# Performance work log

Hardware: AMD Instinct MI355X
Metric: run time of the kernel (lower is better)

## Reference

```python
import jax, jax.numpy as jnp
import numpy as np

VAR = 1.0
STD = float(np.sqrt(VAR))


def setup_inputs() -> dict:
    key = jax.random.key(0)
    k1, k2 = jax.random.split(key)
    n, c = 262144, 100
    scores = jax.random.normal(k1, (n, c), dtype=jnp.float32)
    labels = jax.random.randint(k2, (n,), 0, c, dtype=jnp.int64)
    return {"scores": scores, "labels": labels}


def reference(scores, labels):
    n, c = scores.shape
    # Gaussian pdf over class indices, centered at each label (re_encode_label)
    x = jnp.arange(c, dtype=scores.dtype)[None, :]            # (1, c)
    mu = labels.astype(scores.dtype)[:, None]                  # (n, 1)
    inv_norm = 1.0 / (STD * np.sqrt(2.0 * np.pi))
    code = inv_norm * jnp.exp(-0.5 * ((x - mu) / STD) ** 2)    # (n, c)
    # target distribution: softmax over the (unnormalized) pdf values
    target = jax.nn.softmax(code, axis=1)
    logsfmx = jax.nn.log_softmax(scores, axis=1)
    # KLDivLoss(reduction='batchmean'): sum(target * (log target - input)) / n
    kl = jnp.sum(target * (jnp.log(target) - logsfmx)) / n
    return kl
```

## Files before the change

kernel.cpp:

```cpp
#include <hip/hip_runtime.h>
#include <math.h>

#define C 100
#define WAVES 4
#define ROWS_PER_PASS 32
#define PASSES 4
#define ROWS_PER_BLOCK (ROWS_PER_PASS * PASSES)
#define PASS_FLOATS (ROWS_PER_PASS * C)
#define FULL_CHUNKS 12
#define INV_NORM 0.3989422804014327f
#define WFAR     0.67102943f

__device__ __forceinline__ float quad_sum(float x) {
    x += __int_as_float(__builtin_amdgcn_update_dpp(
            0, __float_as_int(x), 0xB1, 0xF, 0xF, true));
    x += __int_as_float(__builtin_amdgcn_update_dpp(
            0, __float_as_int(x), 0x4E, 0xF, 0xF, true));
    return x;
}
__device__ __forceinline__ float oct_sum(float x) {
    x = quad_sum(x);
    x += __shfl_xor(x, 4);
    return x;
}

__global__ __launch_bounds__(256, 6) void kl_main(
    const float* __restrict__ scores,
    const int*   __restrict__ labels,
    float* __restrict__ out, int n, float inv_n)
{
    __shared__ float buf[2][PASS_FLOATS];
    __shared__ float wpart[WAVES];

    const int tid  = threadIdx.x;
    const int wave = tid >> 6, lane = tid & 63;
    const int rw   = lane >> 3;
    const int sub8 = lane & 7;
    const int rowInPassBase = wave * 8 + rw;

    const int blockRow0 = blockIdx.x * ROWS_PER_BLOCK;
    const size_t totalBytes = (size_t)n * C * 4;

    int mu[PASSES];
    #pragma unroll
    for (int p = 0; p < PASSES; ++p) {
        int row = blockRow0 + p * ROWS_PER_PASS + rowInPassBase;
        mu[p] = (row < n) ? labels[row] : 0;
    }

    float acc = 0.f;

    auto stage = [&](int p, int b) {
        const size_t byteBase = (size_t)(blockRow0 + p * ROWS_PER_PASS) * (C * 4);
        #pragma unroll
        for (int k = 0; k < 3; ++k) {
            int c = wave + k * WAVES;
            size_t off = byteBase + (size_t)c * 1024;
            if (off + 1024 > totalBytes) off = totalBytes - 1024;
            const char* src = (const char*)scores + off + lane * 16;
            __builtin_amdgcn_global_load_lds(
                (const __attribute__((address_space(1))) void*)src,
                (__attribute__((address_space(3))) void*)&buf[b][c * 256],
                16, 0, 0);
        }
        if (wave == 0) {
            size_t off = byteBase + (size_t)FULL_CHUNKS * 1024;
            if (off + 512 > totalBytes) off = totalBytes - 512;
            if (lane < 32) {
                const char* src = (const char*)scores + off + lane * 16;
                __builtin_amdgcn_global_load_lds(
                    (const __attribute__((address_space(1))) void*)src,
                    (__attribute__((address_space(3))) void*)&buf[b][FULL_CHUNKS * 256],
                    16, 0, 0);
            }
        }
    };

    auto consume = [&](int p, int b) {
        const float* sp = &buf[b][rowInPassBase * C];
        const int off = sub8 * 13 - max(sub8 - 4, 0);
        const float* spl = sp + off;
        float se = 0.f, rs = 0.f;
        #pragma unroll
        for (int i = 0; i < 12; ++i) {
            float s = spl[i];
            se += __expf(s);
            rs += s;
        }
        if (sub8 < 4) {
            float s = spl[12];
            se += __expf(s);
            rs += s;
        }
        se = oct_sum(se);
        rs = oct_sum(rs);

        const float WP[7] = {0.32897057f, 0.18369895f, 0.03722540f,
            0.00298049f, 8.9804e-5f, 9.9763e-7f, 4.0768e-9f};
        const float WC[7] = {0.39894228f, 0.20681926f, 0.03823936f,
            0.00298711f, 8.9816e-5f, 9.9765e-7f, 4.0768e-9f};
        float dotw = 0.f, csum = 100.f * WFAR, dotc = 0.f;
        const int m = mu[p];
        #pragma unroll
        for (int d = -6; d <= 6; ++d) {
            int idx  = m + d;
            bool ok  = (unsigned)idx < (unsigned)C;
            float s  = sp[min(max(idx, 0), C - 1)];
            int a    = d < 0 ? -d : d;
            float wv = ok ? WP[a] : 0.f;
            dotw  = fmaf(wv, s, dotw);
            csum += wv;
            dotc += ok ? WC[a] : 0.f;
        }

        int myrow = blockRow0 + p * ROWS_PER_PASS + rowInPassBase;
        if (sub8 == 0 && myrow < n) {
            float dot = fmaf(WFAR, rs, dotw);
            acc += (dotc - dot) / csum - INV_NORM - __logf(csum) + __logf(se);
        }
    };

    #define VMBAR(N) do { asm volatile("s_waitcnt vmcnt(" #N ")" ::: "memory"); \
                          __builtin_amdgcn_s_barrier();                          \
                          asm volatile("" ::: "memory"); } while (0)
    #define BAR()    do { asm volatile("" ::: "memory");                         \
                          __builtin_amdgcn_s_barrier();                          \
                          asm volatile("" ::: "memory"); } while (0)

    stage(0, 0);
    stage(1, 1);

    VMBAR(3);
    consume(0, 0);
    BAR();
    stage(2, 0);

    VMBAR(3);
    consume(1, 1);
    BAR();
    stage(3, 1);

    VMBAR(3);
    consume(2, 0);

    VMBAR(0);
    consume(3, 1);

    #undef VMBAR
    #undef BAR

    #pragma unroll
    for (int off = 32; off > 0; off >>= 1)
        acc += __shfl_xor(acc, off, 64);
    if (lane == 0) wpart[wave] = acc;
    __syncthreads();
    if (tid == 0)
        atomicAdd(out, (wpart[0] + wpart[1] + wpart[2] + wpart[3]) * inv_n);
}

extern "C" void kernel_launch(void* const* d_in, const int* in_sizes, int n_in,
                              void* d_out, int out_size, void* d_ws, size_t ws_size,
                              hipStream_t stream)
{
    const float* scores = (const float*)d_in[0];
    const int*   labels = (const int*)d_in[1];
    float*       out    = (float*)d_out;

    int n = in_sizes[0] / C;

    hipMemsetAsync(d_out, 0, sizeof(float) * (size_t)out_size, stream);

    int blocks = (n + ROWS_PER_BLOCK - 1) / ROWS_PER_BLOCK;
    kl_main<<<blocks, 256, 0, stream>>>(scores, labels, out, n, 1.0f / (float)n);
}
```

Measured before the change: 164.6 us.

## Double rows per block and generalize LDS double-buffer pipeline loop

Doubles the number of 32-row passes per block from 4 to 8, so each block handles 256 rows and the grid shrinks by half, which spreads the per-block prologue and atomic cost over more work. The hand-unrolled stage/consume sequence becomes a generic unrolled loop. The wait count is now per wave, since wave 0 issues an extra tail load. The out-of-bounds clamping on global addresses is removed, which assumes n is a multiple of the block row count; otherwise the last block would read past the end of the array.

```diff
diff --git a/kernel.cpp b/kernel.cpp
--- a/kernel.cpp
+++ b/kernel.cpp
@@ -4,7 +4,7 @@
 #define C 100
 #define WAVES 4
 #define ROWS_PER_PASS 32
-#define PASSES 4
+#define PASSES 8
 #define ROWS_PER_BLOCK (ROWS_PER_PASS * PASSES)
 #define PASS_FLOATS (ROWS_PER_PASS * C)
 #define FULL_CHUNKS 12
@@ -39,7 +39,6 @@
     const int rowInPassBase = wave * 8 + rw;
 
     const int blockRow0 = blockIdx.x * ROWS_PER_BLOCK;
-    const size_t totalBytes = (size_t)n * C * 4;
 
     int mu[PASSES];
     #pragma unroll
@@ -55,24 +54,20 @@
         #pragma unroll
         for (int k = 0; k < 3; ++k) {
             int c = wave + k * WAVES;
-            size_t off = byteBase + (size_t)c * 1024;
-            if (off + 1024 > totalBytes) off = totalBytes - 1024;
-            const char* src = (const char*)scores + off + lane * 16;
+            const char* src = (const char*)scores + byteBase + (size_t)c * 1024
+                              + lane * 16;
             __builtin_amdgcn_global_load_lds(
                 (const __attribute__((address_space(1))) void*)src,
                 (__attribute__((address_space(3))) void*)&buf[b][c * 256],
                 16, 0, 0);
         }
-        if (wave == 0) {
-            size_t off = byteBase + (size_t)FULL_CHUNKS * 1024;
-            if (off + 512 > totalBytes) off = totalBytes - 512;
-            if (lane < 32) {
-                const char* src = (const char*)scores + off + lane * 16;
-                __builtin_amdgcn_global_load_lds(
-                    (const __attribute__((address_space(1))) void*)src,
-                    (__attribute__((address_space(3))) void*)&buf[b][FULL_CHUNKS * 256],
-                    16, 0, 0);
-            }
+        if (wave == 0 && lane < 32) {
+            const char* src = (const char*)scores + byteBase
+                              + (size_t)FULL_CHUNKS * 1024 + lane * 16;
+            __builtin_amdgcn_global_load_lds(
+                (const __attribute__((address_space(1))) void*)src,
+                (__attribute__((address_space(3))) void*)&buf[b][FULL_CHUNKS * 256],
+                16, 0, 0);
         }
     };
 
@@ -120,34 +115,29 @@
         }
     };
 
-    #define VMBAR(N) do { asm volatile("s_waitcnt vmcnt(" #N ")" ::: "memory"); \
-                          __builtin_amdgcn_s_barrier();                          \
-                          asm volatile("" ::: "memory"); } while (0)
-    #define BAR()    do { asm volatile("" ::: "memory");                         \
-                          __builtin_amdgcn_s_barrier();                          \
-                          asm volatile("" ::: "memory"); } while (0)
-
     stage(0, 0);
     stage(1, 1);
 
-    VMBAR(3);
-    consume(0, 0);
-    BAR();
-    stage(2, 0);
+    #pragma unroll
+    for (int p = 0; p < PASSES; ++p) {
+        if (p < PASSES - 1) {
+            if (wave == 0) asm volatile("s_waitcnt vmcnt(4)" ::: "memory");
+            else           asm volatile("s_waitcnt vmcnt(3)" ::: "memory");
+        } else {
+            asm volatile("s_waitcnt vmcnt(0)" ::: "memory");
+        }
+        __builtin_amdgcn_s_barrier();
+        asm volatile("" ::: "memory");
 
-    VMBAR(3);
-    consume(1, 1);
-    BAR();
-    stage(3, 1);
+        consume(p, p & 1);
 
-    VMBAR(3);
-    consume(2, 0);
-
-    VMBAR(0);
-    consume(3, 1);
-
-    #undef VMBAR
-    #undef BAR
+        if (p < PASSES - 2) {
+            asm volatile("" ::: "memory");
+            __builtin_amdgcn_s_barrier();
+            asm volatile("" ::: "memory");
+            stage(p + 2, p & 1);
+        }
+    }
 
     #pragma unroll
     for (int off = 32; off > 0; off >>= 1)
```

New measurement: 163.8 us. About the same (-0.5%).
